# Performance work log

Hardware: AMD Instinct MI355X
Metric: run time of the kernel (lower is better)

Reference implementation:

```python
import jax, jax.numpy as jnp
import numpy as np

B, S, D = 256, 1024, 32   # batch, seq_len, raw feature dim
H, L = 128, 2             # hidden_dim, num_layers
IN = D + 2                # GRU input: features + mask + time-delta


def setup_inputs() -> dict:
    key = jax.random.key(0)
    ks = jax.random.split(key, 16)
    x = jax.random.normal(ks[0], (B, S, D), jnp.float32)
    nan_mask = jax.random.bernoulli(ks[1], 0.3, (B, S))
    x = jnp.where(nan_mask[:, :, None], jnp.nan, x)  # missing timesteps are all-NaN
    # strictly increasing timestamps shared across batch
    t = jnp.cumsum(jax.random.uniform(ks[2], (S,), jnp.float32, 0.1, 1.0))

    def init(k, shape):
        s = 1.0 / np.sqrt(H)
        return jax.random.uniform(k, shape, jnp.float32, -s, s)

    params = {}
    in_dims = [IN, H]
    for l in range(L):
        params[f"Wih{l}"] = init(ks[3 + 4 * l], (3 * H, in_dims[l]))
        params[f"Whh{l}"] = init(ks[4 + 4 * l], (3 * H, H))
        params[f"bih{l}"] = init(ks[5 + 4 * l], (3 * H,))
        params[f"bhh{l}"] = init(ks[6 + 4 * l], (3 * H,))
    return {"t": t, "x": x, **params}


def _impute(t, x):
    # mask[b,i] = 1 if timestep i of sample b is missing (any NaN feature)
    mask = jnp.isnan(x).any(-1)                      # [B,S] bool
    # prev[b,i] = last observed index strictly before i, or -1 (parallel cummax)
    idx = jnp.where(~mask, jnp.arange(S)[None, :], -1)
    cmax = jax.lax.cummax(idx, axis=1)
    prev = jnp.concatenate([jnp.full((B, 1), -1), cmax[:, :-1]], axis=1)  # [B,S]
    prev_c = jnp.clip(prev, 0, S - 1)
    x_clean = jnp.nan_to_num(x)
    x_prev = jnp.take_along_axis(x_clean, prev_c[:, :, None], axis=1)
    # masked: forward-fill from last observation (zeros if none); unmasked: keep x
    imputed = jnp.where(mask[:, :, None],
                        jnp.where((prev >= 0)[:, :, None], x_prev, 0.0),
                        x_clean)
    # time delta: t[i]-t[prev] when a previous observation exists, else raw t delta
    t_deltas = jnp.concatenate([jnp.zeros((1,), t.dtype), t[1:] - t[:-1]])
    t_exp = jnp.where(prev >= 0, t[None, :] - t[prev_c], t_deltas[None, :])  # [B,S]
    return jnp.concatenate([imputed,
                            mask.astype(jnp.float32)[:, :, None],
                            t_exp[:, :, None]], axis=-1)  # [B,S,D+2]


def _gru_layer(xseq, Wih, Whh, bih, bhh):
    # precompute input projections for all timesteps (one big GEMM)
    gx = jnp.einsum('bsd,gd->bsg', xseq, Wih) + bih  # [B,S,3H], gate order r,z,n

    def step(h, g):
        gh = h @ Whh.T + bhh
        r = jax.nn.sigmoid(g[:, :H] + gh[:, :H])
        z = jax.nn.sigmoid(g[:, H:2 * H] + gh[:, H:2 * H])
        n = jnp.tanh(g[:, 2 * H:] + r * gh[:, 2 * H:])
        h = (1.0 - z) * n + z * h
        return h, h

    h0 = jnp.zeros((xseq.shape[0], H), xseq.dtype)
    _, hs = jax.lax.scan(step, h0, gx.transpose(1, 0, 2))
    return hs.transpose(1, 0, 2)  # [B,S,H]


def reference(t, x, Wih0, Whh0, bih0, bhh0, Wih1, Whh1, bih1, bhh1):
    inp = _impute(t, x)
    h = _gru_layer(inp, Wih0, Whh0, bih0, bhh0)
    h = _gru_layer(h, Wih1, Whh1, bih1, bhh1)
    return h[:, -1, :]  # [B,H]
```

## Files before the change

### kernel.cpp

```cpp
#include <hip/hip_runtime.h>


#define BB 256
#define SS 1024
#define DD 32
#define HH 128
#define NT 768

typedef _Float16 f16;
typedef __attribute__((ext_vector_type(2))) _Float16 h2;

__device__ inline h2 as_h2(int x) { union { int i; h2 h; } u; u.i = x; return u.h; }

__device__ inline float dot2(h2 a, h2 b, float c) {
    return __builtin_amdgcn_fdot2(a, b, c, false);
}

__device__ inline float frcp(float x) { return __builtin_amdgcn_rcpf(x); }
__device__ inline float fast_sigm(float x) { return frcp(1.0f + __expf(-x)); }
__device__ inline float fast_tanh(float x) {
    x = fminf(15.0f, fmaxf(-15.0f, x));
    float e = __expf(-2.0f * x);
    return (1.0f - e) * frcp(1.0f + e);
}

struct ImpState { float xprev, tprev; bool hasprev; };

__device__ inline void impute_store(int i, float xv, int l, ImpState& st,
                                    f16* hxs, const float* tb) {
    bool nanp = (l < 32) && (xv != xv);
    unsigned long long bal = __ballot(nanp);
    bool mask = bal != 0ull;
    if (l < 32) {
        float imp = mask ? st.xprev : xv;
        hxs[l] = (f16)imp;
        if (!mask) st.xprev = xv;
    }
    float tcur = tb[i];
    float tdel = (i == 0) ? 0.0f : (tcur - tb[i - 1]);
    float texp = st.hasprev ? (tcur - st.tprev) : tdel;
    if (l == 32) hxs[32] = (f16)(mask ? 1.0f : 0.0f);
    if (l == 33) hxs[33] = (f16)texp;
    if (!mask) { st.hasprev = true; st.tprev = tcur; }
}

__global__
__attribute__((amdgpu_flat_work_group_size(NT, NT), amdgpu_waves_per_eu(3, 3)))
void gru_fused(
    const float* __restrict__ t_in, const float* __restrict__ x_in,
    const float* __restrict__ Wih0, const float* __restrict__ Whh0,
    const float* __restrict__ bih0, const float* __restrict__ bhh0,
    const float* __restrict__ Wih1, const float* __restrict__ Whh1,
    const float* __restrict__ bih1, const float* __restrict__ bhh1,
    float* __restrict__ out, char* __restrict__ ws)
{
    __shared__ float tb[SS];
    __shared__ float2 pA[NT];
    __shared__ float2 pB[NT];
    __shared__ __align__(16) f16 h0s[HH];
    __shared__ __align__(16) f16 h1s[HH];
    __shared__ __align__(16) f16 hxs[48];

    const int tid = threadIdx.x;
    const int b = blockIdx.x;
    const int group = tid >= 384;
    const int row = tid - 384 * group;

    h2 wih0[9], whh0[32], wih1[32], whh1[32];
    {
        const float* p = Wih0 + row * 34;
        const int lim = 8 + group;
        #pragma unroll
        for (int k = 0; k < 9; k++) {
            int e = 16 * group + 2 * k;
            f16 lo = (k < lim) ? (f16)p[e]     : (f16)0.0f;
            f16 hi = (k < lim) ? (f16)p[e + 1] : (f16)0.0f;
            h2 v = {lo, hi}; wih0[k] = v;
        }
        p = Whh0 + row * HH + 64 * group;
        #pragma unroll
        for (int k = 0; k < 32; k++) { h2 v = {(f16)p[2*k], (f16)p[2*k+1]}; whh0[k] = v; }
        p = Wih1 + row * HH + 64 * group;
        #pragma unroll
        for (int k = 0; k < 32; k++) { h2 v = {(f16)p[2*k], (f16)p[2*k+1]}; wih1[k] = v; }
        p = Whh1 + row * HH + 64 * group;
        #pragma unroll
        for (int k = 0; k < 32; k++) { h2 v = {(f16)p[2*k], (f16)p[2*k+1]}; whh1[k] = v; }
    }

    const bool isU = (tid >= 512);
    const bool isU0 = (tid >= 512 && tid < 640);
    const int j = isU0 ? (tid - 512) : (tid - 640);
    float ubi[3], ubh[3]; float hr = 0.0f;
    if (isU) {
        const float* bi = isU0 ? bih0 : bih1;
        const float* bh = isU0 ? bhh0 : bhh1;
        #pragma unroll
        for (int q = 0; q < 3; q++) { ubi[q] = bi[j + 128*q]; ubh[q] = bh[j + 128*q]; }
    }

    for (int i2 = tid; i2 < SS; i2 += NT) tb[i2] = t_in[i2];
    if (tid < 64)        ((int*)h0s)[tid]       = 0;
    else if (tid < 128)  ((int*)h1s)[tid - 64]  = 0;
    else if (tid < 152)  ((int*)hxs)[tid - 128] = 0;

    const float* xrow = x_in + (size_t)b * SS * DD + tid;
    ImpState st; st.xprev = 0.0f; st.tprev = 0.0f; st.hasprev = false;

    __syncthreads();
    if (tid < 64) {
        float xv0 = (tid < 32) ? xrow[0] : 0.0f;
        impute_store(0, xv0, tid, st, hxs, tb);
    }
    __syncthreads();

    const int4* h0v  = (const int4*)(h0s + 64 * group);
    const int4* h1v  = (const int4*)(h1s + 64 * group);
    const int4* hxv4 = (const int4*)(hxs + 16 * group);
    const int*  hxep = (const int*)(hxs + 32);

    for (int i = 0; i <= SS; ++i) {
        const bool doL0 = (i < SS), doL1 = (i > 0), doImp = (i + 1 < SS);

        float xv_n = 0.0f;
        if (tid < 32 && doImp) xv_n = xrow[(size_t)(i + 1) * DD];

        float aP = 0.0f;
        {
            int4 u0 = hxv4[0], u1 = hxv4[1];
            int he = *hxep;
            aP = dot2(as_h2(u0.x), wih0[0], aP);
            aP = dot2(as_h2(u0.y), wih0[1], aP);
            aP = dot2(as_h2(u0.z), wih0[2], aP);
            aP = dot2(as_h2(u0.w), wih0[3], aP);
            aP = dot2(as_h2(u1.x), wih0[4], aP);
            aP = dot2(as_h2(u1.y), wih0[5], aP);
            aP = dot2(as_h2(u1.z), wih0[6], aP);
            aP = dot2(as_h2(u1.w), wih0[7], aP);
            aP = dot2(as_h2(he),   wih0[8], aP);
        }
        float cC[4] = {0,0,0,0}, dC[4] = {0,0,0,0}, eC[4] = {0,0,0,0};
        #pragma unroll
        for (int c = 0; c < 8; ++c) {
            int4 v = h0v[c];
            cC[0] = dot2(as_h2(v.x), whh0[4*c+0], cC[0]);
            dC[0] = dot2(as_h2(v.x), wih1[4*c+0], dC[0]);
            cC[1] = dot2(as_h2(v.y), whh0[4*c+1], cC[1]);
            dC[1] = dot2(as_h2(v.y), wih1[4*c+1], dC[1]);
            cC[2] = dot2(as_h2(v.z), whh0[4*c+2], cC[2]);
            dC[2] = dot2(as_h2(v.z), wih1[4*c+2], dC[2]);
            cC[3] = dot2(as_h2(v.w), whh0[4*c+3], cC[3]);
            dC[3] = dot2(as_h2(v.w), wih1[4*c+3], dC[3]);
        }
        #pragma unroll
        for (int c = 0; c < 8; ++c) {
            int4 v = h1v[c];
            eC[0] = dot2(as_h2(v.x), whh1[4*c+0], eC[0]);
            eC[1] = dot2(as_h2(v.y), whh1[4*c+1], eC[1]);
            eC[2] = dot2(as_h2(v.z), whh1[4*c+2], eC[2]);
            eC[3] = dot2(as_h2(v.w), whh1[4*c+3], eC[3]);
        }
        float cP = (cC[0] + cC[1]) + (cC[2] + cC[3]);
        float dP = (dC[0] + dC[1]) + (dC[2] + dC[3]);
        float eP = (eC[0] + eC[1]) + (eC[2] + eC[3]);
        pA[tid] = make_float2(aP, cP);
        pB[tid] = make_float2(dP, eP);
        __syncthreads();

        if (isU) {
            bool act = isU0 ? doL0 : doL1;
            if (act) {
                const float2* P = isU0 ? pA : pB;
                float2 q0a = P[j],       q0b = P[384 + j];
                float2 q1a = P[j + 128], q1b = P[384 + j + 128];
                float2 q2a = P[j + 256], q2b = P[384 + j + 256];
                float rx = q0a.x + q0b.x, rh = q0a.y + q0b.y;
                float zx = q1a.x + q1b.x, zh = q1a.y + q1b.y;
                float nx = q2a.x + q2b.x, nh = q2a.y + q2b.y;
                float r = fast_sigm(ubi[0] + ubh[0] + rx + rh);
                float z = fast_sigm(ubi[1] + ubh[1] + zx + zh);
                float n = fast_tanh(ubi[2] + nx + r * (ubh[2] + nh));
                hr = (1.0f - z) * n + z * hr;
                f16* hp = isU0 ? h0s : h1s;
                hp[j] = (f16)hr;
            }
        } else if (tid < 64 && doImp) {
            impute_store(i + 1, xv_n, tid, st, hxs, tb);
        }
        __syncthreads();
    }

    if (tid >= 640) out[(size_t)b * HH + (tid - 640)] = hr;
}

extern "C" void kernel_launch(void* const* d_in, const int* in_sizes, int n_in,
                              void* d_out, int out_size, void* d_ws, size_t ws_size,
                              hipStream_t stream) {
    gru_fused<<<dim3(BB), dim3(NT), 0, stream>>>(
        (const float*)d_in[0], (const float*)d_in[1],
        (const float*)d_in[2], (const float*)d_in[3],
        (const float*)d_in[4], (const float*)d_in[5],
        (const float*)d_in[6], (const float*)d_in[7],
        (const float*)d_in[8], (const float*)d_in[9],
        (float*)d_out, (char*)d_ws);
}
```

Baseline: 1.334 ms.

## Give each dot thread full weight rows and shrink block to 512 threads

```diff
diff --git a/kernel.cpp b/kernel.cpp
--- a/kernel.cpp
+++ b/kernel.cpp
@@ -5,7 +5,7 @@
 #define SS 1024
 #define DD 32
 #define HH 128
-#define NT 768
+#define NT 512
 
 typedef _Float16 f16;
 typedef __attribute__((ext_vector_type(2))) _Float16 h2;
@@ -45,7 +45,7 @@
 }
 
 __global__
-__attribute__((amdgpu_flat_work_group_size(NT, NT), amdgpu_waves_per_eu(3, 3)))
+__attribute__((amdgpu_flat_work_group_size(NT, NT), amdgpu_waves_per_eu(2, 2)))
 void gru_fused(
     const float* __restrict__ t_in, const float* __restrict__ x_in,
     const float* __restrict__ Wih0, const float* __restrict__ Whh0,
@@ -54,55 +54,54 @@
     const float* __restrict__ bih1, const float* __restrict__ bhh1,
     float* __restrict__ out, char* __restrict__ ws)
 {
+    __shared__ __align__(16) int v_op[152];
     __shared__ float tb[SS];
-    __shared__ float2 pA[NT];
-    __shared__ float2 pB[NT];
-    __shared__ __align__(16) f16 h0s[HH];
-    __shared__ __align__(16) f16 h1s[HH];
-    __shared__ __align__(16) f16 hxs[48];
+    __shared__ float g0[384], g1[384];
+    __shared__ float g0n[128], g1n[128];
 
     const int tid = threadIdx.x;
     const int b = blockIdx.x;
-    const int group = tid >= 384;
-    const int row = tid - 384 * group;
-
-    h2 wih0[9], whh0[32], wih1[32], whh1[32];
-    {
-        const float* p = Wih0 + row * 34;
-        const int lim = 8 + group;
-        #pragma unroll
-        for (int k = 0; k < 9; k++) {
-            int e = 16 * group + 2 * k;
-            f16 lo = (k < lim) ? (f16)p[e]     : (f16)0.0f;
-            f16 hi = (k < lim) ? (f16)p[e + 1] : (f16)0.0f;
-            h2 v = {lo, hi}; wih0[k] = v;
+    const bool isDot = tid < 384;
+    const bool isU0  = (tid >= 384 && tid < 448);
+    const bool isU1  = tid >= 448;
+    const int r = tid;
+    const int lane = tid & 63;
+
+    h2 w_a[24], w_c[64], w_d[64], w_e[64];
+    if (isDot) {
+        const float* p = Wih0 + r * 34;
+        #pragma unroll
+        for (int k = 0; k < 24; k++) {
+            f16 lo = (k < 17) ? (f16)p[2*k]   : (f16)0.0f;
+            f16 hi = (k < 17) ? (f16)p[2*k+1] : (f16)0.0f;
+            h2 v = {lo, hi}; w_a[k] = v;
         }
-        p = Whh0 + row * HH + 64 * group;
-        #pragma unroll
-        for (int k = 0; k < 32; k++) { h2 v = {(f16)p[2*k], (f16)p[2*k+1]}; whh0[k] = v; }
-        p = Wih1 + row * HH + 64 * group;
-        #pragma unroll
-        for (int k = 0; k < 32; k++) { h2 v = {(f16)p[2*k], (f16)p[2*k+1]}; wih1[k] = v; }
-        p = Whh1 + row * HH + 64 * group;
-        #pragma unroll
-        for (int k = 0; k < 32; k++) { h2 v = {(f16)p[2*k], (f16)p[2*k+1]}; whh1[k] = v; }
-    }
-
-    const bool isU = (tid >= 512);
-    const bool isU0 = (tid >= 512 && tid < 640);
-    const int j = isU0 ? (tid - 512) : (tid - 640);
-    float ubi[3], ubh[3]; float hr = 0.0f;
-    if (isU) {
+        p = Whh0 + r * HH;
+        #pragma unroll
+        for (int k = 0; k < 64; k++) { h2 v = {(f16)p[2*k], (f16)p[2*k+1]}; w_c[k] = v; }
+        p = Wih1 + r * HH;
+        #pragma unroll
+        for (int k = 0; k < 64; k++) { h2 v = {(f16)p[2*k], (f16)p[2*k+1]}; w_d[k] = v; }
+        p = Whh1 + r * HH;
+        #pragma unroll
+        for (int k = 0; k < 64; k++) { h2 v = {(f16)p[2*k], (f16)p[2*k+1]}; w_e[k] = v; }
+    }
+
+    float ubi[3][2], ubh[3][2], hr[2] = {0.0f, 0.0f};
+    if (isU0 || isU1) {
         const float* bi = isU0 ? bih0 : bih1;
         const float* bh = isU0 ? bhh0 : bhh1;
         #pragma unroll
-        for (int q = 0; q < 3; q++) { ubi[q] = bi[j + 128*q]; ubh[q] = bh[j + 128*q]; }
+        for (int q = 0; q < 3; q++)
+            #pragma unroll
+            for (int u = 0; u < 2; u++) {
+                ubi[q][u] = bi[lane + 64*u + 128*q];
+                ubh[q][u] = bh[lane + 64*u + 128*q];
+            }
     }
 
     for (int i2 = tid; i2 < SS; i2 += NT) tb[i2] = t_in[i2];
-    if (tid < 64)        ((int*)h0s)[tid]       = 0;
-    else if (tid < 128)  ((int*)h1s)[tid - 64]  = 0;
-    else if (tid < 152)  ((int*)hxs)[tid - 128] = 0;
+    if (tid < 152) v_op[tid] = 0;
 
     const float* xrow = x_in + (size_t)b * SS * DD + tid;
     ImpState st; st.xprev = 0.0f; st.tprev = 0.0f; st.hasprev = false;
@@ -110,87 +109,89 @@
     __syncthreads();
     if (tid < 64) {
         float xv0 = (tid < 32) ? xrow[0] : 0.0f;
-        impute_store(0, xv0, tid, st, hxs, tb);
+        impute_store(0, xv0, tid, st, (f16*)v_op, tb);
     }
     __syncthreads();
 
-    const int4* h0v  = (const int4*)(h0s + 64 * group);
-    const int4* h1v  = (const int4*)(h1s + 64 * group);
-    const int4* hxv4 = (const int4*)(hxs + 16 * group);
-    const int*  hxep = (const int*)(hxs + 32);
+    const int4* vb = (const int4*)v_op;
+    f16* hf = (f16*)v_op;
 
     for (int i = 0; i <= SS; ++i) {
-        const bool doL0 = (i < SS), doL1 = (i > 0), doImp = (i + 1 < SS);
+        const bool doImp = (i + 1 < SS);
 
         float xv_n = 0.0f;
         if (tid < 32 && doImp) xv_n = xrow[(size_t)(i + 1) * DD];
 
-        float aP = 0.0f;
-        {
-            int4 u0 = hxv4[0], u1 = hxv4[1];
-            int he = *hxep;
-            aP = dot2(as_h2(u0.x), wih0[0], aP);
-            aP = dot2(as_h2(u0.y), wih0[1], aP);
-            aP = dot2(as_h2(u0.z), wih0[2], aP);
-            aP = dot2(as_h2(u0.w), wih0[3], aP);
-            aP = dot2(as_h2(u1.x), wih0[4], aP);
-            aP = dot2(as_h2(u1.y), wih0[5], aP);
-            aP = dot2(as_h2(u1.z), wih0[6], aP);
-            aP = dot2(as_h2(u1.w), wih0[7], aP);
-            aP = dot2(as_h2(he),   wih0[8], aP);
-        }
-        float cC[4] = {0,0,0,0}, dC[4] = {0,0,0,0}, eC[4] = {0,0,0,0};
-        #pragma unroll
-        for (int c = 0; c < 8; ++c) {
-            int4 v = h0v[c];
-            cC[0] = dot2(as_h2(v.x), whh0[4*c+0], cC[0]);
-            dC[0] = dot2(as_h2(v.x), wih1[4*c+0], dC[0]);
-            cC[1] = dot2(as_h2(v.y), whh0[4*c+1], cC[1]);
-            dC[1] = dot2(as_h2(v.y), wih1[4*c+1], dC[1]);
-            cC[2] = dot2(as_h2(v.z), whh0[4*c+2], cC[2]);
-            dC[2] = dot2(as_h2(v.z), wih1[4*c+2], dC[2]);
-            cC[3] = dot2(as_h2(v.w), whh0[4*c+3], cC[3]);
-            dC[3] = dot2(as_h2(v.w), wih1[4*c+3], dC[3]);
-        }
-        #pragma unroll
-        for (int c = 0; c < 8; ++c) {
-            int4 v = h1v[c];
-            eC[0] = dot2(as_h2(v.x), whh1[4*c+0], eC[0]);
-            eC[1] = dot2(as_h2(v.y), whh1[4*c+1], eC[1]);
-            eC[2] = dot2(as_h2(v.z), whh1[4*c+2], eC[2]);
-            eC[3] = dot2(as_h2(v.w), whh1[4*c+3], eC[3]);
-        }
-        float cP = (cC[0] + cC[1]) + (cC[2] + cC[3]);
-        float dP = (dC[0] + dC[1]) + (dC[2] + dC[3]);
-        float eP = (eC[0] + eC[1]) + (eC[2] + eC[3]);
-        pA[tid] = make_float2(aP, cP);
-        pB[tid] = make_float2(dP, eP);
-        __syncthreads();
-
-        if (isU) {
-            bool act = isU0 ? doL0 : doL1;
-            if (act) {
-                const float2* P = isU0 ? pA : pB;
-                float2 q0a = P[j],       q0b = P[384 + j];
-                float2 q1a = P[j + 128], q1b = P[384 + j + 128];
-                float2 q2a = P[j + 256], q2b = P[384 + j + 256];
-                float rx = q0a.x + q0b.x, rh = q0a.y + q0b.y;
-                float zx = q1a.x + q1b.x, zh = q1a.y + q1b.y;
-                float nx = q2a.x + q2b.x, nh = q2a.y + q2b.y;
-                float r = fast_sigm(ubi[0] + ubh[0] + rx + rh);
-                float z = fast_sigm(ubi[1] + ubh[1] + zx + zh);
-                float n = fast_tanh(ubi[2] + nx + r * (ubh[2] + nh));
-                hr = (1.0f - z) * n + z * hr;
-                f16* hp = isU0 ? h0s : h1s;
-                hp[j] = (f16)hr;
-            }
-        } else if (tid < 64 && doImp) {
-            impute_store(i + 1, xv_n, tid, st, hxs, tb);
+        if (isDot) {
+            float accA = 0.0f;
+            #pragma unroll
+            for (int c = 0; c < 6; ++c) {
+                int4 v = vb[c];
+                accA = dot2(as_h2(v.x), w_a[4*c+0], accA);
+                accA = dot2(as_h2(v.y), w_a[4*c+1], accA);
+                accA = dot2(as_h2(v.z), w_a[4*c+2], accA);
+                accA = dot2(as_h2(v.w), w_a[4*c+3], accA);
+            }
+            float c0=0.f,c1=0.f,d0=0.f,d1=0.f,e0=0.f,e1=0.f;
+            #pragma unroll
+            for (int c = 0; c < 16; ++c) {
+                int4 v = vb[6 + c];
+                c0 = dot2(as_h2(v.x), w_c[4*c+0], c0);
+                d0 = dot2(as_h2(v.x), w_d[4*c+0], d0);
+                c1 = dot2(as_h2(v.y), w_c[4*c+1], c1);
+                d1 = dot2(as_h2(v.y), w_d[4*c+1], d1);
+                c0 = dot2(as_h2(v.z), w_c[4*c+2], c0);
+                d0 = dot2(as_h2(v.z), w_d[4*c+2], d0);
+                c1 = dot2(as_h2(v.w), w_c[4*c+3], c1);
+                d1 = dot2(as_h2(v.w), w_d[4*c+3], d1);
+            }
+            #pragma unroll
+            for (int c = 0; c < 16; ++c) {
+                int4 v = vb[22 + c];
+                e0 = dot2(as_h2(v.x), w_e[4*c+0], e0);
+                e1 = dot2(as_h2(v.y), w_e[4*c+1], e1);
+                e0 = dot2(as_h2(v.z), w_e[4*c+2], e0);
+                e1 = dot2(as_h2(v.w), w_e[4*c+3], e1);
+            }
+            float accC = c0 + c1, accD = d0 + d1, accE = e0 + e1;
+            if (r < 256) {
+                g0[r] = accA + accC;
+                g1[r] = accD + accE;
+            } else {
+                g0[r] = accA; g0n[r - 256] = accC;
+                g1[r] = accD; g1n[r - 256] = accE;
+            }
         }
         __syncthreads();
-    }
-
-    if (tid >= 640) out[(size_t)b * HH + (tid - 640)] = hr;
+
+        if (isU0 || isU1) {
+            bool act = isU0 ? (i < SS) : (i > 0);
+            if (act) {
+                const float* G  = isU0 ? g0 : g1;
+                const float* Gn = isU0 ? g0n : g1n;
+                const int hbase = isU0 ? 48 : 176;
+                #pragma unroll
+                for (int u = 0; u < 2; ++u) {
+                    int j = lane + 64*u;
+                    float rg = fast_sigm(G[j]       + ubi[0][u] + ubh[0][u]);
+                    float zg = fast_sigm(G[j + 128] + ubi[1][u] + ubh[1][u]);
+                    float ng = fast_tanh(G[j + 256] + ubi[2][u]
+                                         + rg * (Gn[j] + ubh[2][u]));
+                    float h = (1.0f - zg) * ng + zg * hr[u];
+                    hr[u] = h;
+                    hf[hbase + j] = (f16)h;
+                }
+            }
+        } else if (tid < 64 && doImp) {
+            impute_store(i + 1, xv_n, tid, st, (f16*)v_op, tb);
+        }
+        __syncthreads();
+    }
+
+    if (isU1) {
+        out[(size_t)b * HH + lane]      = hr[0];
+        out[(size_t)b * HH + lane + 64] = hr[1];
+    }
 }
 
 extern "C" void kernel_launch(void* const* d_in, const int* in_sizes, int n_in,
```

After: 2.064 ms. +54.7%, slower.
